# Kernel tuning notes

Hardware: AMD Instinct MI355X
Metric: run time of the kernel (lower is better)

## Reference

```python
import jax, jax.numpy as jnp
import numpy as np

H = 16          # n_heads
DN = 128        # qk_nope_head_dim
DR = 64         # qk_rope_head_dim
DV = 128        # v_head_dim
R = 512         # kv_lora_rank
DIM = 2048
THETA = 10000.0
EPS = 1e-6
SCALE = (DN + DR) ** -0.5


def rms_norm(x, w):
    var = jnp.mean(x * x, axis=-1, keepdims=True)
    return x * jax.lax.rsqrt(var + EPS) * w


def rope_cos_sin(seqlen):
    # DeepSeek freqs: 1/theta^(2i/d) over adjacent pairs
    inv = 1.0 / (THETA ** (jnp.arange(0, DR, 2, dtype=jnp.float32) / DR))  # [DR/2]
    ang = jnp.arange(seqlen, dtype=jnp.float32)[:, None] * inv             # [s, DR/2]
    return jnp.cos(ang), jnp.sin(ang)


def apply_rope(t, cos, sin):
    # t: [b, s, h, DR]; rotate adjacent pairs (complex multiply)
    b, s, h, d = t.shape
    t = t.reshape(b, s, h, d // 2, 2)
    x0, x1 = t[..., 0], t[..., 1]
    c = cos[None, :, None, :]
    sn = sin[None, :, None, :]
    out = jnp.stack([x0 * c - x1 * sn, x0 * sn + x1 * c], axis=-1)
    return out.reshape(b, s, h, d)


def setup_inputs() -> dict:
    key = jax.random.key(0)
    ks = jax.random.split(key, 6)
    b, s = 2, 2048
    sc = lambda n: n ** -0.5
    return {
        "x": jax.random.normal(ks[0], (b, s, DIM), jnp.float32),
        "wq": jax.random.normal(ks[1], (DIM, H * (DN + DR)), jnp.float32) * sc(DIM),
        "wkv_a": jax.random.normal(ks[2], (DIM, R + DR), jnp.float32) * sc(DIM),
        "kv_norm_w": jnp.ones((R,), jnp.float32),
        "wkv_b": jax.random.normal(ks[3], (R, H * (DN + DV)), jnp.float32) * sc(R),
        "wo": jax.random.normal(ks[4], (H * DV, DIM), jnp.float32) * sc(H * DV),
    }


def reference(x, wq, wkv_a, kv_norm_w, wkv_b, wo):
    b, s, _ = x.shape
    cos, sin = rope_cos_sin(s)

    # Query projection (q_lora_rank == 0 -> direct)
    q = (x @ wq).reshape(b, s, H, DN + DR)
    q_nope, q_pe = q[..., :DN], q[..., DN:]
    q_pe = apply_rope(q_pe, cos, sin)

    # Compressed KV + decoupled rope key
    kv_a = x @ wkv_a                      # [b, s, R+DR]
    kv, k_pe = kv_a[..., :R], kv_a[..., R:]
    k_pe = apply_rope(k_pe[:, :, None, :], cos, sin)  # [b, s, 1, DR]
    kv = rms_norm(kv, kv_norm_w)
    kvb = (kv @ wkv_b).reshape(b, s, H, DN + DV)
    k_nope, v = kvb[..., :DN], kvb[..., DN:]

    qf = jnp.concatenate([q_nope, q_pe], axis=-1)                         # [b,s,H,192]
    kf = jnp.concatenate([k_nope, jnp.broadcast_to(k_pe, (b, s, H, DR))], axis=-1)

    scores = jnp.einsum("bshd,bthd->bhst", qf, kf) * SCALE
    mask = jnp.tril(jnp.ones((s, s), bool))
    scores = jnp.where(mask[None, None], scores, jnp.finfo(scores.dtype).min)
    p = jax.nn.softmax(scores, axis=-1)
    out = jnp.einsum("bhst,bthd->bshd", p, v).reshape(b, s, H * DV)
    return out @ wo
```

## Files before the change

### kernel.cpp

```cpp
#include <hip/hip_runtime.h>
#include <hip/hip_bf16.h>
#include <math.h>

#define NB 2
#define NS 2048
#define ND 2048
#define NH 16
#define DNOPE 128
#define DROPE 64
#define DVAL 128
#define RANK 512
#define QW (NH*(DNOPE+DROPE))
#define AW (RANK+DROPE)
#define AWPAD 640
#define BW (NH*(DNOPE+DVAL))
#define OW (NH*DVAL)
#define ATT_SCALE 0.07216878364870322f
#define ATT_SCALE2 0.10411758590510176f

typedef __attribute__((ext_vector_type(8))) short short8;
typedef __attribute__((ext_vector_type(4))) float f32x4;

__device__ __forceinline__ float b2f(unsigned short u) {
  unsigned x = ((unsigned)u) << 16; float f; __builtin_memcpy(&f, &x, 4); return f;
}
__device__ __forceinline__ unsigned short f2b(float f) {
  unsigned x; __builtin_memcpy(&x, &f, 4);
  unsigned r = (x + 0x7fffu + ((x >> 16) & 1u)) >> 16;
  return (unsigned short)r;
}
__device__ __forceinline__ unsigned cvtpk(float a, float b) {
  unsigned r;
  asm("v_cvt_pk_bf16_f32 %0, %1, %2" : "=v"(r) : "v"(a), "v"(b));
  return r;
}
__device__ __forceinline__ void gload16(const void* g, void* lds) {
  __builtin_amdgcn_global_load_lds((const __attribute__((address_space(1))) void*)g,
                                   (__attribute__((address_space(3))) void*)lds, 16, 0, 0);
}

__global__ __launch_bounds__(256) void k_cvt(const float* __restrict__ X,
                                             unsigned short* __restrict__ Y) {
  long i = ((long)blockIdx.x * 256 + threadIdx.x) * 4;
  float4 v = *(const float4*)(X + i);
  ushort4 o;
  o.x = f2b(v.x); o.y = f2b(v.y); o.z = f2b(v.z); o.w = f2b(v.w);
  *(ushort4*)(Y + i) = o;
}

__global__ __launch_bounds__(256) void k_transpose(const float* __restrict__ W,
                                                   unsigned short* __restrict__ WT,
                                                   int K, int N) {
  __shared__ float t[32][33];
  const int k0 = blockIdx.x * 32, n0 = blockIdx.y * 32;
  const int tx = threadIdx.x & 31, ty = threadIdx.x >> 5;
  #pragma unroll
  for (int i = 0; i < 32; i += 8) {
    int n = n0 + tx;
    float v = (n < N) ? W[(size_t)(k0 + ty + i) * N + n] : 0.f;
    t[ty + i][tx] = v;
  }
  __syncthreads();
  #pragma unroll
  for (int i = 0; i < 32; i += 8)
    WT[(size_t)(n0 + ty + i) * K + k0 + tx] = f2b(t[tx][ty + i]);
}

template <typename OutT>
__global__ __launch_bounds__(256) void gemm_bf16(
    const unsigned short* __restrict__ A, const unsigned short* __restrict__ BT,
    OutT* __restrict__ C, int M, int N, int K, int lda) {
  __shared__ short8 AsV[1024];
  __shared__ short8 BsV[1024];
  const int tid = threadIdx.x;
  const int l = tid & 63, w = tid >> 6;
  const int nwg = gridDim.x * gridDim.y;
  const int bid = blockIdx.y * gridDim.x + blockIdx.x;
  const int sbid = (bid & 7) * (nwg >> 3) + (bid >> 3);
  const int bx = sbid % gridDim.x, by = sbid / gridDim.x;
  const int bm = by * 128, bn = bx * 128;
  const int wm = (w >> 1) * 64, wn = (w & 1) * 64;
  f32x4 acc[4][4] = {};

  const int srow = tid >> 3;
  const int gk   = ((((tid & 7) * 16) ^ ((srow & 7) << 4)) >> 1);
  const int sw   = l & 7;

  for (int k0 = 0; k0 < K; k0 += 64) {
    #pragma unroll
    for (int i = 0; i < 4; ++i) {
      const int row = i * 32 + srow;
      gload16(A + (size_t)(bm + row) * lda + k0 + gk, (char*)AsV + i * 4096 + w * 1024);
      gload16(BT + (size_t)(bn + row) * K   + k0 + gk, (char*)BsV + i * 4096 + w * 1024);
    }
    __syncthreads();
    #pragma unroll
    for (int kk2 = 0; kk2 < 2; ++kk2) {
      const int kb = kk2 * 4 + (l >> 4);
      short8 af[4], bg[4];
      #pragma unroll
      for (int mi = 0; mi < 4; ++mi)
        af[mi] = AsV[(wm + mi * 16 + (l & 15)) * 8 + (kb ^ sw)];
      #pragma unroll
      for (int ni = 0; ni < 4; ++ni)
        bg[ni] = BsV[(wn + ni * 16 + (l & 15)) * 8 + (kb ^ sw)];
      #pragma unroll
      for (int mi = 0; mi < 4; ++mi)
        #pragma unroll
        for (int ni = 0; ni < 4; ++ni)
          acc[mi][ni] = __builtin_amdgcn_mfma_f32_16x16x32_bf16(af[mi], bg[ni], acc[mi][ni], 0, 0, 0);
    }
    __syncthreads();
  }

  const int r0 = bm + wm + (l >> 4) * 4;
  const int c0 = bn + wn + (l & 15);
  #pragma unroll
  for (int mi = 0; mi < 4; ++mi)
    #pragma unroll
    for (int ni = 0; ni < 4; ++ni) {
      const int col = c0 + ni * 16;
      if (col < N) {
        #pragma unroll
        for (int j = 0; j < 4; ++j) {
          float v = acc[mi][ni][j];
          if constexpr (__is_same(OutT, float))
            C[(size_t)(r0 + mi * 16 + j) * N + col] = v;
          else
            C[(size_t)(r0 + mi * 16 + j) * N + col] = f2b(v);
        }
      }
    }
}

__global__ __launch_bounds__(256) void gemm_fused_qkva(
    const unsigned short* __restrict__ A, const unsigned short* __restrict__ BT,
    unsigned short* __restrict__ Cq, unsigned short* __restrict__ Ckva, int K) {
  __shared__ short8 AsV[1024];
  __shared__ short8 BsV[1024];
  const int tid = threadIdx.x;
  const int l = tid & 63, w = tid >> 6;
  const int nwg = gridDim.x * gridDim.y;
  const int bid = blockIdx.y * gridDim.x + blockIdx.x;
  const int sbid = (bid & 7) * (nwg >> 3) + (bid >> 3);
  const int bx = sbid % gridDim.x, by = sbid / gridDim.x;
  const int bm = by * 128, bn = bx * 128;
  const int wm = (w >> 1) * 64, wn = (w & 1) * 64;
  f32x4 acc[4][4] = {};

  const int srow = tid >> 3;
  const int gk   = ((((tid & 7) * 16) ^ ((srow & 7) << 4)) >> 1);
  const int sw   = l & 7;

  for (int k0 = 0; k0 < K; k0 += 64) {
    #pragma unroll
    for (int i = 0; i < 4; ++i) {
      const int row = i * 32 + srow;
      gload16(A + (size_t)(bm + row) * K + k0 + gk, (char*)AsV + i * 4096 + w * 1024);
      gload16(BT + (size_t)(bn + row) * K + k0 + gk, (char*)BsV + i * 4096 + w * 1024);
    }
    __syncthreads();
    #pragma unroll
    for (int kk2 = 0; kk2 < 2; ++kk2) {
      const int kb = kk2 * 4 + (l >> 4);
      short8 af[4], bg[4];
      #pragma unroll
      for (int mi = 0; mi < 4; ++mi)
        af[mi] = AsV[(wm + mi * 16 + (l & 15)) * 8 + (kb ^ sw)];
      #pragma unroll
      for (int ni = 0; ni < 4; ++ni)
        bg[ni] = BsV[(wn + ni * 16 + (l & 15)) * 8 + (kb ^ sw)];
      #pragma unroll
      for (int mi = 0; mi < 4; ++mi)
        #pragma unroll
        for (int ni = 0; ni < 4; ++ni)
          acc[mi][ni] = __builtin_amdgcn_mfma_f32_16x16x32_bf16(af[mi], bg[ni], acc[mi][ni], 0, 0, 0);
    }
    __syncthreads();
  }

  const int r0 = bm + wm + (l >> 4) * 4;
  const int c0 = bn + wn + (l & 15);
  #pragma unroll
  for (int mi = 0; mi < 4; ++mi)
    #pragma unroll
    for (int ni = 0; ni < 4; ++ni) {
      const int col = c0 + ni * 16;
      #pragma unroll
      for (int j = 0; j < 4; ++j) {
        const float v = acc[mi][ni][j];
        const int row = r0 + mi * 16 + j;
        if (col < QW)
          Cq[(size_t)row * QW + col] = f2b(v);
        else if (col - QW < AW)
          Ckva[(size_t)row * AW + (col - QW)] = f2b(v);
      }
    }
}

__global__ __launch_bounds__(256) void k_rms_b(unsigned short* __restrict__ kva,
                                               const float* __restrict__ w) {
  const int row = blockIdx.x;
  unsigned short* p = kva + (long)row * AW;
  __shared__ float sd[256];
  float ss = 0.f;
  for (int j = threadIdx.x; j < RANK; j += 256) { float v = b2f(p[j]); ss += v * v; }
  sd[threadIdx.x] = ss;
  __syncthreads();
  for (int st = 128; st > 0; st >>= 1) {
    if (threadIdx.x < st) sd[threadIdx.x] += sd[threadIdx.x + st];
    __syncthreads();
  }
  const float sc = rsqrtf(sd[0] / (float)RANK + 1e-6f);
  for (int j = threadIdx.x; j < RANK; j += 256) p[j] = f2b(b2f(p[j]) * sc * w[j]);
}

__global__ __launch_bounds__(64) void k_ropek_b(unsigned short* __restrict__ kva) {
  const int row = blockIdx.x;
  const int t = row & (NS - 1);
  const int i = threadIdx.x;
  if (i >= 32) return;
  const double invf = pow(10000.0, -(double)i / 32.0);
  const double ang = (double)t * invf;
  const float c = (float)cos(ang), s = (float)sin(ang);
  unsigned short* p = kva + (long)row * AW + RANK + 2 * i;
  const float x0 = b2f(p[0]), x1 = b2f(p[1]);
  p[0] = f2b(x0 * c - x1 * s);
  p[1] = f2b(x0 * s + x1 * c);
}

__global__ __launch_bounds__(512) void k_ropeq_b(unsigned short* __restrict__ q) {
  const int row = blockIdx.x;
  const int t = row & (NS - 1);
  const int h = threadIdx.x >> 5;
  const int i = threadIdx.x & 31;
  const double invf = pow(10000.0, -(double)i / 32.0);
  const double ang = (double)t * invf;
  const float c = (float)cos(ang), s = (float)sin(ang);
  unsigned short* p = q + (long)row * QW + h * (DNOPE + DROPE) + DNOPE + 2 * i;
  const float x0 = b2f(p[0]), x1 = b2f(p[1]);
  p[0] = f2b(x0 * c - x1 * s);
  p[1] = f2b(x0 * s + x1 * c);
}

#define KBLK 64
#define KSL 24
#define VTS 72
#define VBUF (DVAL*VTS)
#define PLS 72
#define QTILES (NS/128)
__global__ __launch_bounds__(512) void k_attn_mfma(
    const unsigned short* __restrict__ qg,
    const unsigned short* __restrict__ kvbg,
    const unsigned short* __restrict__ kvag,
    unsigned short* __restrict__ attg) {
  __shared__ short8 Ks[KBLK * KSL];
  __shared__ __align__(16) unsigned short VT[2 * VBUF];
  __shared__ __align__(16) unsigned short Pl[128 * PLS];
  const int tid = threadIdx.x;
  const int l = tid & 63, w = tid >> 6;
  const int g = l >> 4, r16 = l & 15;
  const int h = blockIdx.y;
  const int b = blockIdx.z;
  const unsigned short* q   = qg   + (size_t)b * NS * QW;
  const unsigned short* kvb = kvbg + (size_t)b * NS * BW;
  const unsigned short* kva = kvag + (size_t)b * NS * AW;
  unsigned short* att = attg + (size_t)b * NS * OW;

  const unsigned short* kbs[3]; int kstp[3]; char* kdst[3];
  #pragma unroll
  for (int i = 0; i < 3; ++i) {
    const int chunk = i * 512 + tid;
    const int row = chunk / KSL, p = chunk % KSL;
    const int s = (p & ~7) | ((p & 7) ^ (row & 7));
    const int d0 = s * 8;
    if (d0 < DNOPE) { kbs[i] = kvb + (size_t)row * BW + h * 256 + d0; kstp[i] = KBLK * BW; }
    else            { kbs[i] = kva + (size_t)row * AW + RANK + (d0 - DNOPE); kstp[i] = KBLK * AW; }
    kdst[i] = (char*)Ks + (size_t)(i * 512 + (tid & ~63)) * 16;
  }
  const int vt_t = tid >> 3, vqd = tid & 7;
  const unsigned short* vbs = kvb + (size_t)vt_t * BW + h * 256 + DNOPE + vqd * 8;
  unsigned short* vwd = VT + (vqd * 8) * VTS + (vt_t ^ (vqd << 3));

  #pragma unroll 1
  for (int phase = 0; phase < 2; ++phase) {
    const int qt = phase ? (QTILES - 1 - (int)blockIdx.x) : (int)blockIdx.x;
    const int nt = 2 * qt + 2;
    const int qrow0 = qt * 128 + w * 16;

    short8 aq[6];
    {
      const unsigned short* qp = q + (size_t)(qrow0 + r16) * QW + h * 192 + g * 8;
      #pragma unroll
      for (int f = 0; f < 6; ++f) aq[f] = *(const short8*)(qp + f * 32);
    }
    f32x4 o[8] = {};
    float m_j[4], l_j[4];
    #pragma unroll
    for (int j = 0; j < 4; ++j) { m_j[j] = -1e30f; l_j[j] = 0.f; }

    const unsigned short* kq0 = kbs[0];
    const unsigned short* kq1 = kbs[1];
    const unsigned short* kq2 = kbs[2];
    const unsigned short* vq  = vbs;

    gload16(kq0, kdst[0]); kq0 += kstp[0];
    gload16(kq1, kdst[1]); kq1 += kstp[1];
    gload16(kq2, kdst[2]); kq2 += kstp[2];
    {
      short8 vA = *(const short8*)(vq);
      short8 vB = *(const short8*)(vq + 64);
      #pragma unroll
      for (int jj = 0; jj < 8; ++jj) {
        vwd[jj * VTS] = (unsigned short)vA[jj];
        vwd[64 * VTS + jj * VTS] = (unsigned short)vB[jj];
      }
      vq += KBLK * BW;
    }
    __syncthreads();
    int cur = 0;

    for (int kt = 0; kt < nt; ++kt) {
      f32x4 sa[4] = {};
      __builtin_amdgcn_s_setprio(1);
      #pragma unroll
      for (int f = 0; f < 6; ++f) {
        #pragma unroll
        for (int n = 0; n < 4; ++n) {
          const int row = n * 16 + r16;
          const int s = f * 4 + g;
          const int phys = (s & ~7) | ((s & 7) ^ (row & 7));
          short8 bg = Ks[row * KSL + phys];
          sa[n] = __builtin_amdgcn_mfma_f32_16x16x32_bf16(aq[f], bg, sa[n], 0, 0, 0);
        }
      }
      __builtin_amdgcn_s_setprio(0);
      __syncthreads();

      const bool pref = (kt + 1 < nt);
      short8 vA, vB;
      if (pref) {
        gload16(kq0, kdst[0]); kq0 += kstp[0];
        gload16(kq1, kdst[1]); kq1 += kstp[1];
        gload16(kq2, kdst[2]); kq2 += kstp[2];
        vA = *(const short8*)(vq);
        vB = *(const short8*)(vq + 64);
        vq += KBLK * BW;
      }

      const bool diag = (kt >= nt - 2);
      float pj[4][4];
      #pragma unroll
      for (int n = 0; n < 4; ++n) {
        const int key = kt * KBLK + n * 16 + r16;
        #pragma unroll
        for (int j = 0; j < 4; ++j) {
          float v = sa[n][j] * ATT_SCALE2;
          if (diag && key > (qrow0 + g * 4 + j)) v = -1e30f;
          pj[n][j] = v;
        }
      }
      float mx4[4];
      float needf = 0.f;
      #pragma unroll
      for (int j = 0; j < 4; ++j) {
        float mx = fmaxf(fmaxf(pj[0][j], pj[1][j]), fmaxf(pj[2][j], pj[3][j]));
        #pragma unroll
        for (int o2 = 1; o2 < 16; o2 <<= 1) mx = fmaxf(mx, __shfl_xor(mx, o2, 64));
        mx4[j] = mx;
        needf += (mx > m_j[j] + 8.f) ? 1.f : 0.f;
      }
      const bool need = __any(needf > 0.f);
      #pragma unroll
      for (int j = 0; j < 4; ++j) {
        if (need) {
          const float mn = fmaxf(m_j[j], mx4[j]);
          const float c = exp2f(m_j[j] - mn);
          l_j[j] *= c;
          #pragma unroll
          for (int n8 = 0; n8 < 8; ++n8) o[n8][j] *= c;
          m_j[j] = mn;
        }
        float rs = 0.f;
        #pragma unroll
        for (int n = 0; n < 4; ++n) {
          float p = exp2f(pj[n][j] - m_j[j]);
          pj[n][j] = p;
          rs += p;
        }
        #pragma unroll
        for (int o2 = 1; o2 < 16; o2 <<= 1) rs += __shfl_xor(rs, o2, 64);
        l_j[j] += rs;
        const int prow = w * 16 + g * 4 + j;
        const unsigned pk01 = cvtpk(pj[0][j], pj[1][j]);
        const unsigned pk23 = cvtpk(pj[2][j], pj[3][j]);
        Pl[prow * PLS +  0 + r16] = (unsigned short)pk01;
        Pl[prow * PLS + 16 + r16] = (unsigned short)(pk01 >> 16);
        Pl[prow * PLS + 32 + r16] = (unsigned short)pk23;
        Pl[prow * PLS + 48 + r16] = (unsigned short)(pk23 >> 16);
      }

      if (pref) {
        unsigned short* dst = vwd + (cur ^ 1) * VBUF;
        #pragma unroll
        for (int jj = 0; jj < 8; ++jj) {
          dst[jj * VTS] = (unsigned short)vA[jj];
          dst[64 * VTS + jj * VTS] = (unsigned short)vB[jj];
        }
      }

      const int hb = r16 >> 3;
      const unsigned short* vbase = VT + cur * VBUF;
      #pragma unroll
      for (int kk = 0; kk < 2; ++kk) {
        short8 pa = *(const short8*)&Pl[(w * 16 + r16) * PLS + kk * 32 + g * 8];
        __builtin_amdgcn_s_setprio(1);
        #pragma unroll
        for (int n8 = 0; n8 < 8; ++n8) {
          const int blk = (kk * 4 + g) ^ ((n8 * 2 + hb) & 7);
          short8 vb = *(const short8*)&vbase[(n8 * 16 + r16) * VTS + blk * 8];
          o[n8] = __builtin_amdgcn_mfma_f32_16x16x32_bf16(pa, vb, o[n8], 0, 0, 0);
        }
        __builtin_amdgcn_s_setprio(0);
      }
      __syncthreads();
      cur ^= 1;
    }

    #pragma unroll
    for (int j = 0; j < 4; ++j) {
      const float inv = 1.0f / l_j[j];
      const size_t rowoff = (size_t)(qrow0 + g * 4 + j) * OW + h * DVAL;
      #pragma unroll
      for (int n8 = 0; n8 < 8; ++n8)
        att[rowoff + n8 * 16 + r16] = f2b(o[n8][j] * inv);
    }
    __syncthreads();
  }
}

extern "C" void kernel_launch(void* const* d_in, const int* in_sizes, int n_in,
                              void* d_out, int out_size, void* d_ws, size_t ws_size,
                              hipStream_t stream) {
  const float* x      = (const float*)d_in[0];
  const float* wq     = (const float*)d_in[1];
  const float* wkv_a  = (const float*)d_in[2];
  const float* w_norm = (const float*)d_in[3];
  const float* wkv_b  = (const float*)d_in[4];
  const float* wo     = (const float*)d_in[5];
  float* out = (float*)d_out;

  unsigned short* wqT   = (unsigned short*)d_ws;
  unsigned short* wkvaT = wqT   + (long)QW * ND;
  unsigned short* wkvbT = wkvaT + (long)AWPAD * ND;
  unsigned short* woT   = wkvbT + (long)BW * RANK;
  unsigned short* xb2   = woT   + (long)ND * OW;
  unsigned short* q2    = xb2   + (long)NB * NS * ND;
  unsigned short* kva2  = q2    + (long)NB * NS * QW;
  unsigned short* kvb2  = kva2  + (long)NB * NS * AW;
  unsigned short* att2  = xb2;

  k_transpose<<<dim3(ND / 32, QW / 32),    dim3(256), 0, stream>>>(wq,    wqT,   ND,  QW);
  k_transpose<<<dim3(ND / 32, AWPAD / 32), dim3(256), 0, stream>>>(wkv_a, wkvaT, ND,  AW);
  k_transpose<<<dim3(RANK / 32, BW / 32),  dim3(256), 0, stream>>>(wkv_b, wkvbT, RANK, BW);
  k_transpose<<<dim3(OW / 32, ND / 32),    dim3(256), 0, stream>>>(wo,    woT,   OW,  ND);

  k_cvt<<<dim3((NB * NS * ND) / 1024), dim3(256), 0, stream>>>(x, xb2);
  gemm_fused_qkva<<<dim3((QW + AWPAD) / 128, (NB * NS) / 128), dim3(256), 0, stream>>>(
      xb2, wqT, q2, kva2, ND);
  k_rms_b<<<dim3(NB * NS), dim3(256), 0, stream>>>(kva2, w_norm);
  k_ropek_b<<<dim3(NB * NS), dim3(64), 0, stream>>>(kva2);
  k_ropeq_b<<<dim3(NB * NS), dim3(512), 0, stream>>>(q2);
  gemm_bf16<unsigned short><<<dim3(BW / 128, (NB * NS) / 128), dim3(256), 0, stream>>>(
      kva2, wkvbT, kvb2, NB * NS, BW, RANK, AW);
  k_attn_mfma<<<dim3(8, NH, NB), dim3(512), 0, stream>>>(q2, kvb2, kva2, att2);
  gemm_bf16<float><<<dim3(ND / 128, (NB * NS) / 128), dim3(256), 0, stream>>>(
      att2, woT, out, NB * NS, ND, OW, OW);
}
```

Before: 342.0 us.

## Shrink attention query tile to 64 rows with 256-thread blocks and single-buffered V

```diff
diff --git a/kernel.cpp b/kernel.cpp
--- a/kernel.cpp
+++ b/kernel.cpp
@@ -246,17 +246,16 @@
 #define KBLK 64
 #define KSL 24
 #define VTS 72
-#define VBUF (DVAL*VTS)
 #define PLS 72
-#define QTILES (NS/128)
-__global__ __launch_bounds__(512) void k_attn_mfma(
+#define QTILES (NS/64)
+__global__ __launch_bounds__(256) void k_attn_mfma(
     const unsigned short* __restrict__ qg,
     const unsigned short* __restrict__ kvbg,
     const unsigned short* __restrict__ kvag,
     unsigned short* __restrict__ attg) {
   __shared__ short8 Ks[KBLK * KSL];
-  __shared__ __align__(16) unsigned short VT[2 * VBUF];
-  __shared__ __align__(16) unsigned short Pl[128 * PLS];
+  __shared__ __align__(16) unsigned short VT[DVAL * VTS];
+  __shared__ __align__(16) unsigned short Pl[64 * PLS];
   const int tid = threadIdx.x;
   const int l = tid & 63, w = tid >> 6;
   const int g = l >> 4, r16 = l & 15;
@@ -267,26 +266,27 @@
   const unsigned short* kva = kvag + (size_t)b * NS * AW;
   unsigned short* att = attg + (size_t)b * NS * OW;
 
-  const unsigned short* kbs[3]; int kstp[3]; char* kdst[3];
+  const unsigned short* kbs[6]; int kstp[6]; char* kdst[6];
   #pragma unroll
-  for (int i = 0; i < 3; ++i) {
-    const int chunk = i * 512 + tid;
+  for (int i = 0; i < 6; ++i) {
+    const int chunk = i * 256 + tid;
     const int row = chunk / KSL, p = chunk % KSL;
     const int s = (p & ~7) | ((p & 7) ^ (row & 7));
     const int d0 = s * 8;
     if (d0 < DNOPE) { kbs[i] = kvb + (size_t)row * BW + h * 256 + d0; kstp[i] = KBLK * BW; }
     else            { kbs[i] = kva + (size_t)row * AW + RANK + (d0 - DNOPE); kstp[i] = KBLK * AW; }
-    kdst[i] = (char*)Ks + (size_t)(i * 512 + (tid & ~63)) * 16;
-  }
-  const int vt_t = tid >> 3, vqd = tid & 7;
-  const unsigned short* vbs = kvb + (size_t)vt_t * BW + h * 256 + DNOPE + vqd * 8;
-  unsigned short* vwd = VT + (vqd * 8) * VTS + (vt_t ^ (vqd << 3));
+    kdst[i] = (char*)Ks + (size_t)(i * 256 + (tid & ~63)) * 16;
+  }
+  const int vt_t = tid >> 2, c4 = tid & 3;
+  const unsigned short* vbs = kvb + (size_t)vt_t * BW + h * 256 + DNOPE + c4 * 8;
+  unsigned short* vwd0 = VT + (c4 * 8) * VTS + (vt_t ^ (c4 << 3));
+  unsigned short* vwd1 = VT + ((c4 + 4) * 8) * VTS + (vt_t ^ ((c4 + 4) << 3));
 
   #pragma unroll 1
   for (int phase = 0; phase < 2; ++phase) {
     const int qt = phase ? (QTILES - 1 - (int)blockIdx.x) : (int)blockIdx.x;
-    const int nt = 2 * qt + 2;
-    const int qrow0 = qt * 128 + w * 16;
+    const int nt = qt + 1;
+    const int qrow0 = qt * 64 + w * 16;
 
     short8 aq[6];
     {
@@ -299,26 +299,32 @@
     #pragma unroll
     for (int j = 0; j < 4; ++j) { m_j[j] = -1e30f; l_j[j] = 0.f; }
 
-    const unsigned short* kq0 = kbs[0];
-    const unsigned short* kq1 = kbs[1];
-    const unsigned short* kq2 = kbs[2];
+    const unsigned short* kq0 = kbs[0]; const unsigned short* kq1 = kbs[1];
+    const unsigned short* kq2 = kbs[2]; const unsigned short* kq3 = kbs[3];
+    const unsigned short* kq4 = kbs[4]; const unsigned short* kq5 = kbs[5];
     const unsigned short* vq  = vbs;
 
     gload16(kq0, kdst[0]); kq0 += kstp[0];
     gload16(kq1, kdst[1]); kq1 += kstp[1];
     gload16(kq2, kdst[2]); kq2 += kstp[2];
+    gload16(kq3, kdst[3]); kq3 += kstp[3];
+    gload16(kq4, kdst[4]); kq4 += kstp[4];
+    gload16(kq5, kdst[5]); kq5 += kstp[5];
     {
-      short8 vA = *(const short8*)(vq);
-      short8 vB = *(const short8*)(vq + 64);
+      short8 v0 = *(const short8*)(vq);
+      short8 v1 = *(const short8*)(vq + 32);
+      short8 v2 = *(const short8*)(vq + 64);
+      short8 v3 = *(const short8*)(vq + 96);
       #pragma unroll
       for (int jj = 0; jj < 8; ++jj) {
-        vwd[jj * VTS] = (unsigned short)vA[jj];
-        vwd[64 * VTS + jj * VTS] = (unsigned short)vB[jj];
+        vwd0[jj * VTS] = (unsigned short)v0[jj];
+        vwd1[jj * VTS] = (unsigned short)v1[jj];
+        vwd0[64 * VTS + jj * VTS] = (unsigned short)v2[jj];
+        vwd1[64 * VTS + jj * VTS] = (unsigned short)v3[jj];
       }
       vq += KBLK * BW;
     }
     __syncthreads();
-    int cur = 0;
 
     for (int kt = 0; kt < nt; ++kt) {
       f32x4 sa[4] = {};
@@ -338,17 +344,22 @@
       __syncthreads();
 
       const bool pref = (kt + 1 < nt);
-      short8 vA, vB;
+      short8 v0, v1, v2, v3;
       if (pref) {
         gload16(kq0, kdst[0]); kq0 += kstp[0];
         gload16(kq1, kdst[1]); kq1 += kstp[1];
         gload16(kq2, kdst[2]); kq2 += kstp[2];
-        vA = *(const short8*)(vq);
-        vB = *(const short8*)(vq + 64);
+        gload16(kq3, kdst[3]); kq3 += kstp[3];
+        gload16(kq4, kdst[4]); kq4 += kstp[4];
+        gload16(kq5, kdst[5]); kq5 += kstp[5];
+        v0 = *(const short8*)(vq);
+        v1 = *(const short8*)(vq + 32);
+        v2 = *(const short8*)(vq + 64);
+        v3 = *(const short8*)(vq + 96);
         vq += KBLK * BW;
       }
 
-      const bool diag = (kt >= nt - 2);
+      const bool diag = (kt == nt - 1);
       float pj[4][4];
       #pragma unroll
       for (int n = 0; n < 4; ++n) {
@@ -400,17 +411,7 @@
         Pl[prow * PLS + 48 + r16] = (unsigned short)(pk23 >> 16);
       }
 
-      if (pref) {
-        unsigned short* dst = vwd + (cur ^ 1) * VBUF;
-        #pragma unroll
-        for (int jj = 0; jj < 8; ++jj) {
-          dst[jj * VTS] = (unsigned short)vA[jj];
-          dst[64 * VTS + jj * VTS] = (unsigned short)vB[jj];
-        }
-      }
-
       const int hb = r16 >> 3;
-      const unsigned short* vbase = VT + cur * VBUF;
       #pragma unroll
       for (int kk = 0; kk < 2; ++kk) {
         short8 pa = *(const short8*)&Pl[(w * 16 + r16) * PLS + kk * 32 + g * 8];
@@ -418,13 +419,22 @@
         #pragma unroll
         for (int n8 = 0; n8 < 8; ++n8) {
           const int blk = (kk * 4 + g) ^ ((n8 * 2 + hb) & 7);
-          short8 vb = *(const short8*)&vbase[(n8 * 16 + r16) * VTS + blk * 8];
+          short8 vb = *(const short8*)&VT[(n8 * 16 + r16) * VTS + blk * 8];
           o[n8] = __builtin_amdgcn_mfma_f32_16x16x32_bf16(pa, vb, o[n8], 0, 0, 0);
         }
         __builtin_amdgcn_s_setprio(0);
       }
       __syncthreads();
-      cur ^= 1;
+
+      if (pref) {
+        #pragma unroll
+        for (int jj = 0; jj < 8; ++jj) {
+          vwd0[jj * VTS] = (unsigned short)v0[jj];
+          vwd1[jj * VTS] = (unsigned short)v1[jj];
+          vwd0[64 * VTS + jj * VTS] = (unsigned short)v2[jj];
+          vwd1[64 * VTS + jj * VTS] = (unsigned short)v3[jj];
+        }
+      }
     }
 
     #pragma unroll
@@ -473,7 +483,7 @@
   k_ropeq_b<<<dim3(NB * NS), dim3(512), 0, stream>>>(q2);
   gemm_bf16<unsigned short><<<dim3(BW / 128, (NB * NS) / 128), dim3(256), 0, stream>>>(
       kva2, wkvbT, kvb2, NB * NS, BW, RANK, AW);
-  k_attn_mfma<<<dim3(8, NH, NB), dim3(512), 0, stream>>>(q2, kvb2, kva2, att2);
+  k_attn_mfma<<<dim3(QTILES / 2, NH, NB), dim3(256), 0, stream>>>(q2, kvb2, kva2, att2);
   gemm_bf16<float><<<dim3(ND / 128, (NB * NS) / 128), dim3(256), 0, stream>>>(
       att2, woT, out, NB * NS, ND, OW, OW);
 }
```

After: 420.5 us. +22.9%, slower.
